# Performance work log

Measured on AMD Instinct MI355X. Metric: run time of the kernel, lower is better.

## Reference

```python
import jax, jax.numpy as jnp
import numpy as np

B_SZ, D, H, W = 32, 96, 64, 64
N = 4            # d_state
R = 6            # dt_rank = ceil(96/16)
K = 5            # d_conv
EPS = 1e-9
LOG_EPS = float(np.log(EPS))


def setup_inputs() -> dict:
    key = jax.random.key(0)
    ks = jax.random.split(key, 8)
    x = jax.random.normal(ks[0], (B_SZ, D, H, W), dtype=jnp.float32)
    conv_w = jax.random.normal(ks[1], (D, 1, K, K), dtype=jnp.float32) * (1.0 / K)
    conv_b = jax.random.normal(ks[2], (D,), dtype=jnp.float32) * 0.02
    x_proj_w = jax.random.normal(ks[3], (R + 2 * N, D), dtype=jnp.float32) * (D ** -0.5)
    dt_w = jax.random.uniform(ks[4], (D, R), dtype=jnp.float32, minval=-(R ** -0.5), maxval=R ** -0.5)
    # dt bias init: inverse-softplus of dt ~ U(log 1e-3, log 1e-1)
    dt = jnp.exp(jax.random.uniform(ks[5], (D,), dtype=jnp.float32) * (np.log(0.1) - np.log(0.001)) + np.log(0.001))
    dt = jnp.clip(dt, 1e-4, None)
    dt_b = dt + jnp.log(-jnp.expm1(-dt))
    A_logs = jnp.log(jnp.broadcast_to(jnp.arange(1, N + 1, dtype=jnp.float32), (D, N)))
    Ds = jnp.ones((D,), dtype=jnp.float32)
    return {"x": x, "conv_w": conv_w, "conv_b": conv_b, "x_proj_w": x_proj_w,
            "dt_w": dt_w, "dt_b": dt_b, "A_logs": A_logs, "Ds": Ds}


def _forward(x, conv_w, conv_b, x_proj_w, dt_w, dt_b, A_logs, Ds):
    B, C, h, w = x.shape
    L = h * w
    # depthwise conv2d, padding='same' for odd kernel, + SiLU
    x = jax.lax.conv_general_dilated(
        x, conv_w, window_strides=(1, 1), padding=((K // 2, K // 2), (K // 2, K // 2)),
        dimension_numbers=("NCHW", "OIHW", "NCHW"), feature_group_count=C)
    x = x + conv_b[None, :, None, None]
    x = jax.nn.silu(x)
    xs = x.reshape(B, C, L)                                  # [B, D, L]
    x_dbl = jnp.einsum("kd,bdl->bkl", x_proj_w, xs)          # [B, R+2N, L]
    dts, Bs, Cs = x_dbl[:, :R], x_dbl[:, R:R + N], x_dbl[:, R + N:]
    delta = jax.nn.softplus(jnp.einsum("dr,brl->bdl", dt_w, dts) + dt_b[None, :, None])
    A = -jnp.exp(A_logs)                                     # [D, N]
    # log(dA.clamp(min=EPS)) with dA = exp(delta * A)  ==  max(delta*A, log EPS)
    log_dA = jnp.maximum(delta[:, :, None, :] * A[None, :, :, None], LOG_EPS)  # [B,D,N,L]
    P = jnp.exp(jnp.cumsum(log_dA, axis=-1))                 # [B,D,N,L]
    dB_u = delta[:, :, None, :] * Bs[:, None, :, :] * xs[:, :, None, :]        # [B,D,N,L]
    hs = P * jnp.cumsum(dB_u / jnp.maximum(P, EPS), axis=-1)  # state trajectory
    y = jnp.einsum("bdnl,bnl->bdl", hs, Cs) + xs * Ds[None, :, None]
    return y.reshape(B, C, h, w)


def reference(x, conv_w, conv_b, x_proj_w, dt_w, dt_b, A_logs, Ds):
    return _forward(x, conv_w, conv_b, x_proj_w, dt_w, dt_b, A_logs, Ds)
```

## Files before the change

### kernel.cpp

```cpp
#include <hip/hip_runtime.h>

#define B_SZ 32
#define D_CH 96
#define L_SZ 4096
#define N_ST 4
#define R_RK 6

static __device__ __forceinline__ float softplus_f(float v) {
    return fmaxf(v, 0.0f) + __logf(1.0f + __expf(-fabsf(v)));
}

#define TS 76
__global__ __launch_bounds__(256) void conv_silu_kernel(
    const float* __restrict__ x, const float* __restrict__ conv_w,
    const float* __restrict__ conv_b, float* __restrict__ xs)
{
    __shared__ float tile[68 * TS];
    const int t = threadIdx.x;
    const int bd = blockIdx.x;
    const int d = bd % D_CH;
    const float* img = x + bd * L_SZ;

    float wreg[25];
#pragma unroll
    for (int i = 0; i < 25; ++i) wreg[i] = conv_w[d * 25 + i];
    const float bias = conv_b[d];

    const float4 z4 = make_float4(0.f, 0.f, 0.f, 0.f);
    for (int i = t; i < 68 * TS / 4; i += 256) ((float4*)tile)[i] = z4;
    __syncthreads();
    for (int i = t; i < 1024; i += 256) {
        const int r = i >> 4;
        const int c = (i & 15) << 2;
        const float4 v = *(const float4*)(img + (r << 6) + c);
        *(float4*)(tile + (r + 2) * TS + 4 + c) = v;
    }
    __syncthreads();

    const int hr = t >> 2;
    const int cb = (t & 3) << 4;

    float acc[16];
#pragma unroll
    for (int j = 0; j < 16; ++j) acc[j] = bias;

#pragma unroll
    for (int kh = 0; kh < 5; ++kh) {
        const float* rp = tile + (hr + kh) * TS + cb;
        float r24[24];
#pragma unroll
        for (int q = 0; q < 6; ++q) {
            const float4 v = ((const float4*)rp)[q];
            r24[4*q+0] = v.x; r24[4*q+1] = v.y; r24[4*q+2] = v.z; r24[4*q+3] = v.w;
        }
#pragma unroll
        for (int j = 0; j < 16; ++j)
#pragma unroll
            for (int kw = 0; kw < 5; ++kw)
                acc[j] += wreg[kh * 5 + kw] * r24[j + kw + 2];
    }

    float* out = xs + bd * L_SZ + (hr << 6) + cb;
#pragma unroll
    for (int q = 0; q < 4; ++q) {
        float4 v;
#pragma unroll
        for (int j = 0; j < 4; ++j) {
            const float a = acc[4*q + j];
            const float s = __builtin_amdgcn_rcpf(1.0f + __expf(-a));
            (&v.x)[j] = a * s;
        }
        ((float4*)out)[q] = v;
    }
}

__global__ __launch_bounds__(256) void proj_kernel(
    const float* __restrict__ xs, const float* __restrict__ x_proj_w,
    float* __restrict__ x_dbl)
{
    __shared__ float red[4][14][64];
    const int t = threadIdx.x;
    const int g = t >> 6;
    const int ll = t & 63;
    const int bi = blockIdx.x;
    const int b = bi >> 6;
    const int chunk = bi & 63;
    const int l = (chunk << 6) + ll;
    const int d0 = __builtin_amdgcn_readfirstlane(g * 24);

    const float* xsb = xs + (b * D_CH + d0) * L_SZ + l;
    float acc[14];
#pragma unroll
    for (int k = 0; k < 14; ++k) acc[k] = 0.0f;

#pragma unroll
    for (int dd = 0; dd < 24; ++dd) {
        const float xv = xsb[dd * L_SZ];
#pragma unroll
        for (int k = 0; k < 14; ++k)
            acc[k] += x_proj_w[k * D_CH + d0 + dd] * xv;
    }

#pragma unroll
    for (int k = 0; k < 14; ++k) red[g][k][ll] = acc[k];
    __syncthreads();

    float* outb = x_dbl + b * 14 * L_SZ + (chunk << 6);
    for (int i = t; i < 14 * 64; i += 256) {
        const int k = i >> 6;
        const int c = i & 63;
        outb[k * L_SZ + c] = red[0][k][c] + red[1][k][c] + red[2][k][c] + red[3][k][c];
    }
}

static __device__ __forceinline__ float block_excl_scan(float v, float* slot, int t)
{
    const int lane = t & 63;
    const int wid = t >> 6;
    float incl = v;
#pragma unroll
    for (int off = 1; off < 64; off <<= 1) {
        const float u = __shfl_up(incl, (unsigned)off, 64);
        if (lane >= off) incl += u;
    }
    if (lane == 63) slot[wid] = incl;
    float ex = __shfl_up(incl, 1u, 64);
    if (lane == 0) ex = 0.0f;
    __syncthreads();
    float wp = 0.0f;
#pragma unroll
    for (int w = 0; w < 7; ++w)
        if (w < wid) wp += slot[w];
    return wp + ex;
}

__global__ __launch_bounds__(512, 4) void scan_kernel(
    const float* __restrict__ xs, const float* __restrict__ x_dbl,
    const float* __restrict__ dt_w, const float* __restrict__ dt_b,
    const float* __restrict__ A_logs, const float* __restrict__ Ds,
    float* __restrict__ y)
{
    constexpr float LOG_EPS_F = -20.723265836946414f;

    __shared__ float slots[8][8];
    const int t = threadIdx.x;
    const int bd = blockIdx.x;
    const int b = bd / D_CH;
    const int d = bd - b * D_CH;
    const int l0 = t * 8;

    const float* xs_row = xs + bd * L_SZ + l0;
    const float* xd = x_dbl + b * 14 * L_SZ + l0;

    float xv[8], dl[8], yac[8];
#pragma unroll
    for (int i = 0; i < 2; ++i) {
        const float4 v = ((const float4*)xs_row)[i];
        xv[4*i+0] = v.x; xv[4*i+1] = v.y; xv[4*i+2] = v.z; xv[4*i+3] = v.w;
    }

    const float dtb = dt_b[d];
#pragma unroll
    for (int i = 0; i < 8; ++i) { dl[i] = dtb; yac[i] = 0.0f; }
#pragma unroll
    for (int r = 0; r < R_RK; ++r) {
        const float wr = dt_w[d * R_RK + r];
        const float* row = xd + r * L_SZ;
#pragma unroll
        for (int i = 0; i < 2; ++i) {
            const float4 v = ((const float4*)row)[i];
            dl[4*i+0] += wr * v.x; dl[4*i+1] += wr * v.y;
            dl[4*i+2] += wr * v.z; dl[4*i+3] += wr * v.w;
        }
    }
#pragma unroll
    for (int i = 0; i < 8; ++i) dl[i] = softplus_f(dl[i]);

    for (int n = 0; n < N_ST; ++n) {
        const float An = -__expf(A_logs[d * N_ST + n]);

        float SP[8];
        float run = 0.0f;
#pragma unroll
        for (int i = 0; i < 8; ++i) {
            run += fmaxf(dl[i] * An, LOG_EPS_F);
            SP[i] = run;
        }
        const float ex1 = block_excl_scan(run, slots[2*n], t);

        const float* Brow = xd + (R_RK + n) * L_SZ;
        float carr[8];
        float run2 = 0.0f;
#pragma unroll
        for (int i = 0; i < 2; ++i) {
            const float4 v = ((const float4*)Brow)[i];
            const float bb[4] = {v.x, v.y, v.z, v.w};
#pragma unroll
            for (int j = 0; j < 4; ++j) {
                const int idx = 4*i + j;
                const float S = SP[idx] + ex1;
                const float e = __expf(-S);
                const float pinv = fminf(e, 1e9f);
                SP[idx] = __builtin_amdgcn_rcpf(e);
                run2 += dl[idx] * bb[j] * xv[idx] * pinv;
                carr[idx] = run2;
            }
        }
        const float ex2 = block_excl_scan(run2, slots[2*n+1], t);

        const float* Crow = xd + (R_RK + N_ST + n) * L_SZ;
#pragma unroll
        for (int i = 0; i < 2; ++i) {
            const float4 v = ((const float4*)Crow)[i];
            const float cc[4] = {v.x, v.y, v.z, v.w};
#pragma unroll
            for (int j = 0; j < 4; ++j) {
                const int idx = 4*i + j;
                yac[idx] += (SP[idx] * (carr[idx] + ex2)) * cc[j];
            }
        }
    }

    const float dsd = Ds[d];
    float* yrow = y + bd * L_SZ + l0;
#pragma unroll
    for (int i = 0; i < 2; ++i) {
        float4 v;
        v.x = yac[4*i+0] + xv[4*i+0] * dsd;
        v.y = yac[4*i+1] + xv[4*i+1] * dsd;
        v.z = yac[4*i+2] + xv[4*i+2] * dsd;
        v.w = yac[4*i+3] + xv[4*i+3] * dsd;
        ((float4*)yrow)[i] = v;
    }
}

extern "C" void kernel_launch(void* const* d_in, const int* in_sizes, int n_in,
                              void* d_out, int out_size, void* d_ws, size_t ws_size,
                              hipStream_t stream)
{
    const float* x        = (const float*)d_in[0];
    const float* conv_w   = (const float*)d_in[1];
    const float* conv_b   = (const float*)d_in[2];
    const float* x_proj_w = (const float*)d_in[3];
    const float* dt_w     = (const float*)d_in[4];
    const float* dt_b     = (const float*)d_in[5];
    const float* A_logs   = (const float*)d_in[6];
    const float* Ds       = (const float*)d_in[7];

    float* y     = (float*)d_out;
    float* xs    = y;
    float* x_dbl = (float*)d_ws;

    conv_silu_kernel<<<B_SZ * D_CH, 256, 0, stream>>>(x, conv_w, conv_b, xs);
    proj_kernel<<<B_SZ * 64, 256, 0, stream>>>(xs, x_proj_w, x_dbl);
    scan_kernel<<<B_SZ * D_CH, 512, 0, stream>>>(xs, x_dbl, dt_w, dt_b,
                                                 A_logs, Ds, y);
}
```

Before: 89.05 us.

## Batch first-pass scans across states and use DPP wave scans in SSM scan

Replaces the shuffle-based block scan with a DPP row/broadcast inclusive scan. The four cumulative log-decay scans are batched so they share a single shared-memory exchange and barrier, which cuts block barriers from eight to five. Exponentials move to the base-2 domain via the native exp2 builtin, and dl*xv and the Ds term are precomputed. The cost is recomputing the decay running sum in the second pass, plus reliance on the DPP control encodings being correct for wave64.

```diff
diff --git a/kernel.cpp b/kernel.cpp
--- a/kernel.cpp
+++ b/kernel.cpp
@@ -8,6 +8,31 @@
 
 static __device__ __forceinline__ float softplus_f(float v) {
     return fmaxf(v, 0.0f) + __logf(1.0f + __expf(-fabsf(v)));
+}
+
+static __device__ __forceinline__ float exp2_fast(float x) {
+#if __has_builtin(__builtin_amdgcn_exp2f)
+    return __builtin_amdgcn_exp2f(x);
+#else
+    return __expf(x * 0.6931471805599453f);
+#endif
+}
+
+template<int CTRL, int RMASK>
+static __device__ __forceinline__ float dpp_add(float v) {
+    const int t = __builtin_amdgcn_update_dpp(0, __float_as_int(v),
+                                              CTRL, RMASK, 0xf, true);
+    return v + __int_as_float(t);
+}
+
+static __device__ __forceinline__ float wave_incl_scan(float v) {
+    v = dpp_add<0x111, 0xf>(v);
+    v = dpp_add<0x112, 0xf>(v);
+    v = dpp_add<0x114, 0xf>(v);
+    v = dpp_add<0x118, 0xf>(v);
+    v = dpp_add<0x142, 0xa>(v);
+    v = dpp_add<0x143, 0xc>(v);
+    return v;
 }
 
 #define TS 76
@@ -113,37 +138,21 @@
     }
 }
 
-static __device__ __forceinline__ float block_excl_scan(float v, float* slot, int t)
-{
-    const int lane = t & 63;
-    const int wid = t >> 6;
-    float incl = v;
-#pragma unroll
-    for (int off = 1; off < 64; off <<= 1) {
-        const float u = __shfl_up(incl, (unsigned)off, 64);
-        if (lane >= off) incl += u;
-    }
-    if (lane == 63) slot[wid] = incl;
-    float ex = __shfl_up(incl, 1u, 64);
-    if (lane == 0) ex = 0.0f;
-    __syncthreads();
-    float wp = 0.0f;
-#pragma unroll
-    for (int w = 0; w < 7; ++w)
-        if (w < wid) wp += slot[w];
-    return wp + ex;
-}
-
 __global__ __launch_bounds__(512, 4) void scan_kernel(
     const float* __restrict__ xs, const float* __restrict__ x_dbl,
     const float* __restrict__ dt_w, const float* __restrict__ dt_b,
     const float* __restrict__ A_logs, const float* __restrict__ Ds,
     float* __restrict__ y)
 {
-    constexpr float LOG_EPS_F = -20.723265836946414f;
-
-    __shared__ float slots[8][8];
-    const int t = threadIdx.x;
+    constexpr float L2EPS = -29.897352853986263f;
+    constexpr float L2E   = 1.4426950408889634f;
+
+    __shared__ float4 s1[8];
+    __shared__ float  s2[N_ST][8];
+
+    const int t    = threadIdx.x;
+    const int lane = t & 63;
+    const int wid  = t >> 6;
     const int bd = blockIdx.x;
     const int b = bd / D_CH;
     const int d = bd - b * D_CH;
@@ -152,7 +161,7 @@
     const float* xs_row = xs + bd * L_SZ + l0;
     const float* xd = x_dbl + b * 14 * L_SZ + l0;
 
-    float xv[8], dl[8], yac[8];
+    float xv[8];
 #pragma unroll
     for (int i = 0; i < 2; ++i) {
         const float4 v = ((const float4*)xs_row)[i];
@@ -160,8 +169,9 @@
     }
 
     const float dtb = dt_b[d];
-#pragma unroll
-    for (int i = 0; i < 8; ++i) { dl[i] = dtb; yac[i] = 0.0f; }
+    float dl[8];
+#pragma unroll
+    for (int i = 0; i < 8; ++i) dl[i] = dtb;
 #pragma unroll
     for (int r = 0; r < R_RK; ++r) {
         const float wr = dt_w[d * R_RK + r];
@@ -176,20 +186,50 @@
 #pragma unroll
     for (int i = 0; i < 8; ++i) dl[i] = softplus_f(dl[i]);
 
+    const float dsd = Ds[d];
+    float dlxv[8], yac[8];
+#pragma unroll
+    for (int i = 0; i < 8; ++i) { dlxv[i] = dl[i] * xv[i]; yac[i] = xv[i] * dsd; }
+
+    float An2[N_ST];
+#pragma unroll
+    for (int n = 0; n < N_ST; ++n)
+        An2[n] = -__expf(A_logs[d * N_ST + n]) * L2E;
+
+    float exw1[N_ST];
+    float4 w4;
+#pragma unroll
     for (int n = 0; n < N_ST; ++n) {
-        const float An = -__expf(A_logs[d * N_ST + n]);
-
-        float SP[8];
         float run = 0.0f;
 #pragma unroll
-        for (int i = 0; i < 8; ++i) {
-            run += fmaxf(dl[i] * An, LOG_EPS_F);
-            SP[i] = run;
-        }
-        const float ex1 = block_excl_scan(run, slots[2*n], t);
-
+        for (int i = 0; i < 8; ++i) run += fmaxf(dl[i] * An2[n], L2EPS);
+        const float incl = wave_incl_scan(run);
+        exw1[n] = incl - run;
+        (&w4.x)[n] = incl;
+    }
+    if (lane == 63) s1[wid] = w4;
+    __syncthreads();
+
+    float ex1[N_ST];
+    {
+        float4 wp = make_float4(0.f, 0.f, 0.f, 0.f);
+#pragma unroll
+        for (int w = 0; w < 7; ++w)
+            if (w < wid) {
+                const float4 v = s1[w];
+                wp.x += v.x; wp.y += v.y; wp.z += v.z; wp.w += v.w;
+            }
+        ex1[0] = wp.x + exw1[0]; ex1[1] = wp.y + exw1[1];
+        ex1[2] = wp.z + exw1[2]; ex1[3] = wp.w + exw1[3];
+    }
+
+#pragma unroll
+    for (int n = 0; n < N_ST; ++n) {
         const float* Brow = xd + (R_RK + n) * L_SZ;
-        float carr[8];
+        const float* Crow = xd + (R_RK + N_ST + n) * L_SZ;
+
+        float carr[8], P[8];
+        float run  = ex1[n];
         float run2 = 0.0f;
 #pragma unroll
         for (int i = 0; i < 2; ++i) {
@@ -198,38 +238,41 @@
 #pragma unroll
             for (int j = 0; j < 4; ++j) {
                 const int idx = 4*i + j;
-                const float S = SP[idx] + ex1;
-                const float e = __expf(-S);
+                run += fmaxf(dl[idx] * An2[n], L2EPS);
+                const float e = exp2_fast(-run);
                 const float pinv = fminf(e, 1e9f);
-                SP[idx] = __builtin_amdgcn_rcpf(e);
-                run2 += dl[idx] * bb[j] * xv[idx] * pinv;
+                P[idx] = __builtin_amdgcn_rcpf(e);
+                run2 = fmaf(dlxv[idx] * bb[j], pinv, run2);
                 carr[idx] = run2;
             }
         }
-        const float ex2 = block_excl_scan(run2, slots[2*n+1], t);
-
-        const float* Crow = xd + (R_RK + N_ST + n) * L_SZ;
-#pragma unroll
-        for (int i = 0; i < 2; ++i) {
-            const float4 v = ((const float4*)Crow)[i];
-            const float cc[4] = {v.x, v.y, v.z, v.w};
-#pragma unroll
-            for (int j = 0; j < 4; ++j) {
-                const int idx = 4*i + j;
-                yac[idx] += (SP[idx] * (carr[idx] + ex2)) * cc[j];
-            }
-        }
-    }
-
-    const float dsd = Ds[d];
+
+        const float4 c0 = ((const float4*)Crow)[0];
+        const float4 c1 = ((const float4*)Crow)[1];
+
+        const float incl = wave_incl_scan(run2);
+        const float exw2 = incl - run2;
+        if (lane == 63) s2[n][wid] = incl;
+        __syncthreads();
+
+        float wp2 = 0.0f;
+#pragma unroll
+        for (int w = 0; w < 7; ++w)
+            if (w < wid) wp2 += s2[n][w];
+        const float ex2 = wp2 + exw2;
+
+        const float cc[8] = {c0.x, c0.y, c0.z, c0.w, c1.x, c1.y, c1.z, c1.w};
+#pragma unroll
+        for (int i = 0; i < 8; ++i)
+            yac[i] = fmaf(P[i] * (carr[i] + ex2), cc[i], yac[i]);
+    }
+
     float* yrow = y + bd * L_SZ + l0;
 #pragma unroll
     for (int i = 0; i < 2; ++i) {
         float4 v;
-        v.x = yac[4*i+0] + xv[4*i+0] * dsd;
-        v.y = yac[4*i+1] + xv[4*i+1] * dsd;
-        v.z = yac[4*i+2] + xv[4*i+2] * dsd;
-        v.w = yac[4*i+3] + xv[4*i+3] * dsd;
+        v.x = yac[4*i+0]; v.y = yac[4*i+1];
+        v.z = yac[4*i+2]; v.w = yac[4*i+3];
         ((float4*)yrow)[i] = v;
     }
 }
```

After: 111.1 us. 1.25x slower.
